# Performance work log

Measured on AMD Instinct MI355X. Metric: run time of the kernel, lower is better.

The kernel has to match this reference:

```python
import jax, jax.numpy as jnp
import numpy as np

D_MODEL = 1024
N_HEADS = 16
D_K = D_MODEL // N_HEADS
D_FF = 4096
EPS = 1e-6


def setup_inputs() -> dict:
    key = jax.random.key(0)
    ks = jax.random.split(key, 12)
    s = 1.0 / np.sqrt(D_MODEL)
    inp = {
        "x": jax.random.normal(ks[0], (4, 2048, D_MODEL), jnp.float32),
        "src_mask": jnp.ones((4, 1, 1, 2048), jnp.int32),
        "Wq": jax.random.normal(ks[1], (D_MODEL, D_MODEL), jnp.float32) * s,
        "bq": jnp.zeros((D_MODEL,), jnp.float32),
        "Wk": jax.random.normal(ks[2], (D_MODEL, D_MODEL), jnp.float32) * s,
        "bk": jnp.zeros((D_MODEL,), jnp.float32),
        "Wv": jax.random.normal(ks[3], (D_MODEL, D_MODEL), jnp.float32) * s,
        "bv": jnp.zeros((D_MODEL,), jnp.float32),
        "Wo": jax.random.normal(ks[4], (D_MODEL, D_MODEL), jnp.float32) * s,
        "bo": jnp.zeros((D_MODEL,), jnp.float32),
        "W1": jax.random.normal(ks[5], (D_MODEL, D_FF), jnp.float32) * s,
        "b1": jnp.zeros((D_FF,), jnp.float32),
        "W2": jax.random.normal(ks[6], (D_FF, D_MODEL), jnp.float32) * (1.0 / np.sqrt(D_FF)),
        "b2": jnp.zeros((D_MODEL,), jnp.float32),
        # scalar LayerNormalization params (alpha=ones(1), bias=zeros(1)) for the 2 residual norms
        "ln1_alpha": jnp.ones((1,), jnp.float32),
        "ln1_bias": jnp.zeros((1,), jnp.float32),
        "ln2_alpha": jnp.ones((1,), jnp.float32),
        "ln2_bias": jnp.zeros((1,), jnp.float32),
    }
    return inp


def _layernorm(x, alpha, bias):
    # matches torch: mean + std (unbiased, ddof=1), (x-mean)/(std+eps)
    mean = jnp.mean(x, axis=-1, keepdims=True)
    std = jnp.std(x, axis=-1, keepdims=True, ddof=1)
    return alpha * ((x - mean) / (std + EPS)) + bias


def _mha(x, mask, Wq, bq, Wk, bk, Wv, bv, Wo, bo):
    B, S, _ = x.shape
    q = (x @ Wq + bq).reshape(B, S, N_HEADS, D_K).transpose(0, 2, 1, 3)
    k = (x @ Wk + bk).reshape(B, S, N_HEADS, D_K).transpose(0, 2, 1, 3)
    v = (x @ Wv + bv).reshape(B, S, N_HEADS, D_K).transpose(0, 2, 1, 3)
    scores = jnp.einsum("bhqd,bhkd->bhqk", q, k) / jnp.sqrt(jnp.float32(D_K))
    scores = jnp.where(mask == 0, jnp.float32(-1e9), scores)
    attn = jax.nn.softmax(scores, axis=-1)
    ctx = jnp.einsum("bhqk,bhkd->bhqd", attn, v)
    ctx = ctx.transpose(0, 2, 1, 3).reshape(B, S, D_MODEL)
    return ctx @ Wo + bo


def reference(x, src_mask, Wq, bq, Wk, bk, Wv, bv, Wo, bo, W1, b1, W2, b2,
              ln1_alpha, ln1_bias, ln2_alpha, ln2_bias):
    # pre-norm residual 1: self-attention
    h = _layernorm(x, ln1_alpha, ln1_bias)
    x = x + _mha(h, src_mask, Wq, bq, Wk, bk, Wv, bv, Wo, bo)
    # pre-norm residual 2: FFN
    h = _layernorm(x, ln2_alpha, ln2_bias)
    ff = jax.nn.relu(h @ W1 + b1) @ W2 + b2
    return x + ff
```

## Files before the change

kernel.cpp:

```cpp
#include <hip/hip_runtime.h>

typedef __attribute__((ext_vector_type(8))) short v8s;
typedef __attribute__((ext_vector_type(4))) short v4s;
typedef __attribute__((ext_vector_type(8))) unsigned short v8u;
typedef __attribute__((ext_vector_type(4))) unsigned short v4u;
typedef __attribute__((ext_vector_type(4))) float f32x4;

#define DEV __device__ __forceinline__

DEV unsigned short f2bf(float f) {
  union { float f; unsigned u; } v; v.f = f;
  unsigned r = v.u + 0x7fffu + ((v.u >> 16) & 1u);
  return (unsigned short)(r >> 16);
}

DEV void gload16(const unsigned short* g, unsigned short* l) {
  __builtin_amdgcn_global_load_lds(
      (const __attribute__((address_space(1))) unsigned int*)g,
      (__attribute__((address_space(3))) unsigned int*)l, 16, 0, 0);
}

__global__ __launch_bounds__(256) void ln_kernel(
    const float* __restrict__ x, unsigned short* __restrict__ h,
    const float* __restrict__ alpha, const float* __restrict__ beta)
{
  int row = blockIdx.x;
  int tid = threadIdx.x;
  const float4* xr = reinterpret_cast<const float4*>(x + (size_t)row * 1024);
  float4 v = xr[tid];
  float s  = v.x + v.y + v.z + v.w;
  float ss = v.x * v.x + v.y * v.y + v.z * v.z + v.w * v.w;
#pragma unroll
  for (int off = 1; off < 64; off <<= 1) {
    s  += __shfl_xor(s, off);
    ss += __shfl_xor(ss, off);
  }
  __shared__ float ps[4][2];
  int wid = tid >> 6, lane = tid & 63;
  if (lane == 0) { ps[wid][0] = s; ps[wid][1] = ss; }
  __syncthreads();
  s  = ps[0][0] + ps[1][0] + ps[2][0] + ps[3][0];
  ss = ps[0][1] + ps[1][1] + ps[2][1] + ps[3][1];
  float mean = s * (1.0f / 1024.0f);
  float var  = (ss - 1024.0f * mean * mean) * (1.0f / 1023.0f);
  float inv  = 1.0f / (sqrtf(fmaxf(var, 0.0f)) + 1e-6f);
  float a = alpha[0], b = beta[0];
  v4u o;
  o[0] = f2bf(a * ((v.x - mean) * inv) + b);
  o[1] = f2bf(a * ((v.y - mean) * inv) + b);
  o[2] = f2bf(a * ((v.z - mean) * inv) + b);
  o[3] = f2bf(a * ((v.w - mean) * inv) + b);
  *reinterpret_cast<v4u*>(h + (size_t)row * 1024 + tid * 4) = o;
}

__global__ __launch_bounds__(256) void transpose_convert(
    const float* __restrict__ W, unsigned short* __restrict__ Wt, int K, int N)
{
  __shared__ float t[32][33];
  int n0 = blockIdx.x * 32, k0 = blockIdx.y * 32;
  int tx = threadIdx.x, ty = threadIdx.y;
#pragma unroll
  for (int i = 0; i < 4; ++i)
    t[ty + i * 8][tx] = W[(size_t)(k0 + ty + i * 8) * N + n0 + tx];
  __syncthreads();
#pragma unroll
  for (int i = 0; i < 4; ++i)
    Wt[(size_t)(n0 + ty + i * 8) * K + k0 + tx] = f2bf(t[tx][ty + i * 8]);
}

enum { MODE_QK = 0, MODE_VT = 1, MODE_RES = 2, MODE_FFN1 = 3 };

#define BUF_ELEMS ((128 + 256) * 64)

DEV void stage_part(const unsigned short* Aptr, const unsigned short* Bptr,
                    unsigned short* buf, int K, int part, int wid, int lane)
{
  {
    int d = (part * 8 + wid) * 64 + lane;
    int r = d >> 3, p = d & 7;
    gload16(Aptr + (size_t)r * K + 8 * (p ^ (r & 7)),
            buf + (size_t)(part * 8 + wid) * 512);
  }
#pragma unroll
  for (int j = 0; j < 2; ++j) {
    int ib = part * 2 + j;
    int d = (ib * 8 + wid) * 64 + lane;
    int r = d >> 3, p = d & 7;
    gload16(Bptr + (size_t)r * K + 8 * (p ^ (r & 7)),
            buf + 128 * 64 + (size_t)(ib * 8 + wid) * 512);
  }
}

template <int MODE>
__global__ __launch_bounds__(512, 2) void gemm_pipe(
    const unsigned short* __restrict__ A, const unsigned short* __restrict__ Bt,
    const float* __restrict__ bias, const float* __restrict__ resid,
    void* __restrict__ out, int M, int N, int K)
{
  __shared__ unsigned short lds[3 * BUF_ELEMS];

  int nbx = M >> 7, nwg = gridDim.x;
  int lin = blockIdx.x;
  int qq = nwg >> 3, rr = nwg & 7;
  int xcd = lin & 7, idx = lin >> 3;
  int swz = (xcd < rr ? xcd * (qq + 1) : rr * (qq + 1) + (xcd - rr) * qq) + idx;
  int bx = swz % nbx, by = swz / nbx;

  int tid = threadIdx.x, lane = tid & 63, wid = tid >> 6;
  int wm = wid >> 2, wn = wid & 3;
  int g = lane >> 4, c0 = lane & 15;
  int rowBase = bx * 128, colBase = by * 256;

  const unsigned short* Ab = A  + (size_t)rowBase * K;
  const unsigned short* Bb = Bt + (size_t)colBase * K;
  int NT = K >> 6;

  f32x4 acc[4][4];
#pragma unroll
  for (int m = 0; m < 4; ++m)
#pragma unroll
    for (int n = 0; n < 4; ++n) acc[m][n] = (f32x4){0.f, 0.f, 0.f, 0.f};

  stage_part(Ab, Bb, lds, K, 0, wid, lane);
  stage_part(Ab, Bb, lds, K, 1, wid, lane);
  stage_part(Ab + 64, Bb + 64, lds + BUF_ELEMS, K, 0, wid, lane);
  stage_part(Ab + 64, Bb + 64, lds + BUF_ELEMS, K, 1, wid, lane);
  asm volatile("s_waitcnt vmcnt(6)" ::: "memory");
  __builtin_amdgcn_s_barrier();
  asm volatile("" ::: "memory");

  int cur = 0;
  for (int t = 0; t < NT; ++t) {
    const char* Abuf = (const char*)(lds + cur * BUF_ELEMS);
    const char* Bbuf = Abuf + 128 * 128;
    int nxt2 = cur + 2; if (nxt2 >= 3) nxt2 -= 3;
    unsigned short* sbuf = lds + nxt2 * BUF_ELEMS;
    bool doStage = (t + 2 < NT);
    int ks = (t + 2) << 6;
    int e = (c0 & 7) << 4;

#pragma unroll
    for (int ph = 0; ph < 2; ++ph) {
      v8s af[4], bfr[4];
#pragma unroll
      for (int m = 0; m < 4; ++m)
        af[m] = *reinterpret_cast<const v8s*>(
            Abuf + (wm * 64 + m * 16 + c0) * 128 + ((ph * 64 + g * 16) ^ e));
#pragma unroll
      for (int n = 0; n < 4; ++n)
        bfr[n] = *reinterpret_cast<const v8s*>(
            Bbuf + (wn * 64 + n * 16 + c0) * 128 + ((ph * 64 + g * 16) ^ e));

      if (doStage) stage_part(Ab + ks, Bb + ks, sbuf, K, ph, wid, lane);

      __builtin_amdgcn_s_setprio(1);
#pragma unroll
      for (int m = 0; m < 4; ++m)
#pragma unroll
        for (int n = 0; n < 4; ++n)
          acc[m][n] = __builtin_amdgcn_mfma_f32_16x16x32_bf16(
              af[m], bfr[n], acc[m][n], 0, 0, 0);
      __builtin_amdgcn_s_setprio(0);

      if (ph == 1) {
        if (doStage) asm volatile("s_waitcnt vmcnt(6)" ::: "memory");
        else         asm volatile("s_waitcnt vmcnt(0)" ::: "memory");
      }
      __builtin_amdgcn_sched_barrier(0);
      __builtin_amdgcn_s_barrier();
      asm volatile("" ::: "memory");
    }
    cur = cur + 1; if (cur >= 3) cur -= 3;
  }

#pragma unroll
  for (int mf = 0; mf < 4; ++mf) {
#pragma unroll
    for (int n = 0; n < 4; ++n) {
#pragma unroll
      for (int r = 0; r < 4; ++r) {
        int row = rowBase + wm * 64 + mf * 16 + g * 4 + r;
        int col = colBase + wn * 64 + n * 16 + c0;
        float v = acc[mf][n][r] + bias[col];
        if constexpr (MODE == MODE_QK) {
          int b = row >> 11, sI = row & 2047, hh = col >> 6, d = col & 63;
          ((unsigned short*)out)[(((size_t)(b * 16 + hh)) * 2048 + sI) * 64 + d] = f2bf(v);
        } else if constexpr (MODE == MODE_VT) {
          int b = row >> 11, sI = row & 2047, hh = col >> 6, d = col & 63;
          ((unsigned short*)out)[(((size_t)(b * 16 + hh)) * 64 + d) * 2048 + sI] = f2bf(v);
        } else if constexpr (MODE == MODE_RES) {
          ((float*)out)[(size_t)row * N + col] = resid[(size_t)row * N + col] + v;
        } else {
          ((unsigned short*)out)[(size_t)row * N + col] = f2bf(fmaxf(v, 0.0f));
        }
      }
    }
  }
}

DEV void writeV(unsigned short* Vbuf, int idx, v8u vv) {
  int d = idx >> 3, k0 = (idx & 7) * 8;
  int slot0 = ((k0 >> 5) << 5) + (((k0 >> 2) & 3) << 3) + (((k0 >> 4) & 1) << 2);
  int b0 = (slot0 * 2) ^ ((d & 7) << 4);
  char* base = (char*)(Vbuf + d * 64);
  v4u lo = {vv[0], vv[1], vv[2], vv[3]};
  v4u hi = {vv[4], vv[5], vv[6], vv[7]};
  *reinterpret_cast<v4u*>(base + b0) = lo;
  *reinterpret_cast<v4u*>(base + (b0 ^ 16)) = hi;
}

__global__ __launch_bounds__(256) void attn_kernel(
    const unsigned short* __restrict__ q, const unsigned short* __restrict__ k,
    const unsigned short* __restrict__ vT, const int* __restrict__ mask,
    unsigned short* __restrict__ ctx)
{
  const int S = 2048, DK = 64, KVB = 64, NT = 32;
  const float SL2E = 0.125f * 1.44269504088896f;
  int bh = blockIdx.x;
  int b = bh >> 4, hh = bh & 15;
  int qbase = blockIdx.y * 64;
  int tid = threadIdx.x, lane = tid & 63, wid = tid >> 6;
  int g = lane >> 4, c0 = lane & 15;

  __shared__ unsigned short Ks[2][KVB * DK];
  __shared__ unsigned short Vs[2][DK * KVB];
  __shared__ float Msf[2][KVB];

  const unsigned short* qb = q  + (size_t)bh * S * DK;
  const unsigned short* kb = k  + (size_t)bh * S * DK;
  const unsigned short* vb = vT + (size_t)bh * DK * S;
  const int* mb = mask + b * S;

  int qrow = qbase + wid * 16 + c0;
  v8s aq[2];
#pragma unroll
  for (int t = 0; t < 2; ++t)
    aq[t] = *reinterpret_cast<const v8s*>(&qb[(size_t)qrow * DK + t * 32 + g * 8]);

  int i0 = tid, i1 = tid + 256;
  int r0 = i0 >> 3, m0 = i0 & 7;
  int r1 = i1 >> 3, m1 = i1 & 7;

  f32x4 acc[4];
#pragma unroll
  for (int no = 0; no < 4; ++no) acc[no] = (f32x4){0.f, 0.f, 0.f, 0.f};
  float mrow = -1e30f, lrow = 0.f;

  {
    gload16(kb + (size_t)r0 * DK + 8 * (m0 ^ (r0 & 7)), &Ks[0][i0 * 8]);
    gload16(kb + (size_t)r1 * DK + 8 * (m1 ^ (r1 & 7)), &Ks[0][i1 * 8]);
    v8u vv0 = *reinterpret_cast<const v8u*>(&vb[(size_t)r0 * S + m0 * 8]);
    v8u vv1 = *reinterpret_cast<const v8u*>(&vb[(size_t)r1 * S + m1 * 8]);
    writeV(Vs[0], i0, vv0);
    writeV(Vs[0], i1, vv1);
    if (tid < KVB) Msf[0][tid] = mb[tid] ? 0.f : -1e9f;
    __syncthreads();
  }

  for (int t = 0; t < NT; ++t) {
    int cur = t & 1, nxt = cur ^ 1;
    int ktn = (t + 1) * KVB;
    bool more = (t + 1 < NT);
    v8u vv0, vv1; float msv = 0.f;
    if (more) {
      gload16(kb + (size_t)(ktn + r0) * DK + 8 * (m0 ^ (r0 & 7)), &Ks[nxt][i0 * 8]);
      gload16(kb + (size_t)(ktn + r1) * DK + 8 * (m1 ^ (r1 & 7)), &Ks[nxt][i1 * 8]);
      vv0 = *reinterpret_cast<const v8u*>(&vb[(size_t)r0 * S + ktn + m0 * 8]);
      vv1 = *reinterpret_cast<const v8u*>(&vb[(size_t)r1 * S + ktn + m1 * 8]);
      if (tid < KVB) msv = mb[ktn + tid] ? 0.f : -1e9f;
    }

    float p[16];
#pragma unroll
    for (int n = 0; n < 4; ++n) {
      f32x4 sa = (f32x4){0.f, 0.f, 0.f, 0.f};
      int kvr = n * 16 + c0;
      const char* krow = (const char*)&Ks[cur][kvr * DK];
      int sw = (kvr & 7) << 4;
#pragma unroll
      for (int tt = 0; tt < 2; ++tt) {
        v8s ak = *reinterpret_cast<const v8s*>(krow + ((tt * 64 + g * 16) ^ sw));
        sa = __builtin_amdgcn_mfma_f32_16x16x32_bf16(ak, aq[tt], sa, 0, 0, 0);
      }
      f32x4 bn = *reinterpret_cast<const f32x4*>(&Msf[cur][n * 16 + g * 4]);
#pragma unroll
      for (int r = 0; r < 4; ++r) p[n * 4 + r] = sa[r] * SL2E + bn[r];
    }

    float pmax = p[0];
#pragma unroll
    for (int i = 1; i < 16; ++i) pmax = fmaxf(pmax, p[i]);
    pmax = fmaxf(pmax, __shfl_xor(pmax, 16));
    pmax = fmaxf(pmax, __shfl_xor(pmax, 32));
    if (!__all(pmax - mrow <= 8.0f)) {
      float mn = fmaxf(mrow, pmax);
      float sc = exp2f(mrow - mn);
      lrow *= sc;
#pragma unroll
      for (int no = 0; no < 4; ++no) {
        acc[no][0] *= sc; acc[no][1] *= sc; acc[no][2] *= sc; acc[no][3] *= sc;
      }
      mrow = mn;
    }
    float ts = 0.f;
#pragma unroll
    for (int i = 0; i < 16; ++i) { p[i] = exp2f(p[i] - mrow); ts += p[i]; }
    ts += __shfl_xor(ts, 16);
    ts += __shfl_xor(ts, 32);
    lrow += ts;

    v8s pbv[2];
#pragma unroll
    for (int c = 0; c < 2; ++c) {
      union { v8s s; unsigned u[4]; } pk;
#pragma unroll
      for (int hph = 0; hph < 4; ++hph)
        asm("v_cvt_pk_bf16_f32 %0, %1, %2"
            : "=v"(pk.u[hph]) : "v"(p[c * 8 + 2 * hph]), "v"(p[c * 8 + 2 * hph + 1]));
      pbv[c] = pk.s;
    }

#pragma unroll
    for (int c = 0; c < 2; ++c) {
#pragma unroll
      for (int no = 0; no < 4; ++no) {
        int d = no * 16 + c0;
        v8s av = *reinterpret_cast<const v8s*>(
            (const char*)&Vs[cur][d * 64] + ((c * 64 + g * 16) ^ ((d & 7) << 4)));
        acc[no] = __builtin_amdgcn_mfma_f32_16x16x32_bf16(av, pbv[c], acc[no], 0, 0, 0);
      }
    }

    if (more) {
      writeV(Vs[nxt], i0, vv0);
      writeV(Vs[nxt], i1, vv1);
      if (tid < KVB) Msf[nxt][tid] = msv;
    }
    __syncthreads();
  }

  float inv = 1.0f / fmaxf(lrow, 1e-20f);
#pragma unroll
  for (int no = 0; no < 4; ++no) {
    v4u o;
    o[0] = f2bf(acc[no][0] * inv);
    o[1] = f2bf(acc[no][1] * inv);
    o[2] = f2bf(acc[no][2] * inv);
    o[3] = f2bf(acc[no][3] * inv);
    *reinterpret_cast<v4u*>(
        &ctx[(size_t)(b * S + qrow) * 1024 + hh * 64 + no * 16 + g * 4]) = o;
  }
}

extern "C" void kernel_launch(void* const* d_in, const int* in_sizes, int n_in,
                              void* d_out, int out_size, void* d_ws, size_t ws_size,
                              hipStream_t stream)
{
  (void)in_sizes; (void)n_in; (void)out_size; (void)ws_size;
  const float* x    = (const float*)d_in[0];
  const int*   mask = (const int*)d_in[1];
  const float* Wq = (const float*)d_in[2];  const float* bq = (const float*)d_in[3];
  const float* Wk = (const float*)d_in[4];  const float* bk = (const float*)d_in[5];
  const float* Wv = (const float*)d_in[6];  const float* bv = (const float*)d_in[7];
  const float* Wo = (const float*)d_in[8];  const float* bo = (const float*)d_in[9];
  const float* W1 = (const float*)d_in[10]; const float* b1 = (const float*)d_in[11];
  const float* W2 = (const float*)d_in[12]; const float* b2 = (const float*)d_in[13];
  const float* ln1a = (const float*)d_in[14]; const float* ln1b = (const float*)d_in[15];
  const float* ln2a = (const float*)d_in[16]; const float* ln2b = (const float*)d_in[17];

  char* ws = (char*)d_ws;
  const size_t MB = (size_t)1 << 20;
  unsigned short* wqT = (unsigned short*)(ws + 0 * MB);
  unsigned short* wkT = (unsigned short*)(ws + 2 * MB);
  unsigned short* wvT = (unsigned short*)(ws + 4 * MB);
  unsigned short* woT = (unsigned short*)(ws + 6 * MB);
  unsigned short* w1T = (unsigned short*)(ws + 8 * MB);
  unsigned short* w2T = (unsigned short*)(ws + 16 * MB);
  unsigned short* hb  = (unsigned short*)(ws + 24 * MB);
  unsigned short* qb  = (unsigned short*)(ws + 40 * MB);
  unsigned short* kb  = (unsigned short*)(ws + 56 * MB);
  unsigned short* vTb = (unsigned short*)(ws + 72 * MB);
  unsigned short* ctx = (unsigned short*)(ws + 88 * MB);
  unsigned short* gb  = (unsigned short*)(ws + 40 * MB);
  float* xout = (float*)d_out;

  dim3 tb(32, 8);
  transpose_convert<<<dim3(32, 32),  tb, 0, stream>>>(Wq, wqT, 1024, 1024);
  transpose_convert<<<dim3(32, 32),  tb, 0, stream>>>(Wk, wkT, 1024, 1024);
  transpose_convert<<<dim3(32, 32),  tb, 0, stream>>>(Wv, wvT, 1024, 1024);
  transpose_convert<<<dim3(32, 32),  tb, 0, stream>>>(Wo, woT, 1024, 1024);
  transpose_convert<<<dim3(128, 32), tb, 0, stream>>>(W1, w1T, 1024, 4096);
  transpose_convert<<<dim3(32, 128), tb, 0, stream>>>(W2, w2T, 4096, 1024);

  ln_kernel<<<8192, 256, 0, stream>>>(x, hb, ln1a, ln1b);

  gemm_pipe<MODE_QK><<<256, 512, 0, stream>>>(hb, wqT, bq, nullptr, qb,  8192, 1024, 1024);
  gemm_pipe<MODE_QK><<<256, 512, 0, stream>>>(hb, wkT, bk, nullptr, kb,  8192, 1024, 1024);
  gemm_pipe<MODE_VT><<<256, 512, 0, stream>>>(hb, wvT, bv, nullptr, vTb, 8192, 1024, 1024);

  attn_kernel<<<dim3(64, 32), 256, 0, stream>>>(qb, kb, vTb, mask, ctx);

  gemm_pipe<MODE_RES><<<256, 512, 0, stream>>>(ctx, woT, bo, x, xout, 8192, 1024, 1024);

  ln_kernel<<<8192, 256, 0, stream>>>(xout, hb, ln2a, ln2b);

  gemm_pipe<MODE_FFN1><<<1024, 512, 0, stream>>>(hb, w1T, b1, nullptr, gb, 8192, 4096, 1024);
  gemm_pipe<MODE_RES><<<256, 512, 0, stream>>>(gb, w2T, b2, xout, xout, 8192, 1024, 4096);
}
```

Measured before the change: 448.7 us.

## Fuse QKV projections, switch GEMMs to 4-stage ring, pre-pack V and fold softmax scale

Replaces the three Q/K/V GEMMs with one fused GEMM over a concatenated weight, using a new 4-deep ring-buffered GEMM with K-step 32 and optional 256-row tiles for the QKV and FFN1 GEMMs. The QKV epilogue folds the softmax scale into Q and writes V in a pre-swizzled per-tile layout, so attention can load V straight into LDS with async loads instead of register shuffles. Attention also skips mask arithmetic when a whole 64-key tile is unmasked. Larger tiles raise register pressure and the epilogue scatter is more complex.

```diff
diff --git a/kernel.cpp b/kernel.cpp
--- a/kernel.cpp
+++ b/kernel.cpp
@@ -1,7 +1,6 @@
 #include <hip/hip_runtime.h>
 
 typedef __attribute__((ext_vector_type(8))) short v8s;
-typedef __attribute__((ext_vector_type(4))) short v4s;
 typedef __attribute__((ext_vector_type(8))) unsigned short v8u;
 typedef __attribute__((ext_vector_type(4))) unsigned short v4u;
 typedef __attribute__((ext_vector_type(4))) float f32x4;
@@ -19,6 +18,8 @@
       (const __attribute__((address_space(1))) unsigned int*)g,
       (__attribute__((address_space(3))) unsigned int*)l, 16, 0, 0);
 }
+
+#define SL2E 0.1803368801111204f
 
 __global__ __launch_bounds__(256) void ln_kernel(
     const float* __restrict__ x, unsigned short* __restrict__ h,
@@ -68,38 +69,25 @@
     Wt[(size_t)(n0 + ty + i * 8) * K + k0 + tx] = f2bf(t[tx][ty + i * 8]);
 }
 
-enum { MODE_QK = 0, MODE_VT = 1, MODE_RES = 2, MODE_FFN1 = 3 };
-
-#define BUF_ELEMS ((128 + 256) * 64)
-
-DEV void stage_part(const unsigned short* Aptr, const unsigned short* Bptr,
-                    unsigned short* buf, int K, int part, int wid, int lane)
+enum { MODE_QKV = 0, MODE_RES = 2, MODE_FFN1 = 3 };
+
+template <int MODE, int BM>
+__global__ __launch_bounds__(512, 2) void gemm_ring(
+    const unsigned short* __restrict__ A, const unsigned short* __restrict__ Bt,
+    const float* __restrict__ bias0, const float* __restrict__ bias1,
+    const float* __restrict__ bias2, const float* __restrict__ resid,
+    void* __restrict__ o0, void* __restrict__ o1, void* __restrict__ o2,
+    int M, int N, int K)
 {
-  {
-    int d = (part * 8 + wid) * 64 + lane;
-    int r = d >> 3, p = d & 7;
-    gload16(Aptr + (size_t)r * K + 8 * (p ^ (r & 7)),
-            buf + (size_t)(part * 8 + wid) * 512);
-  }
-#pragma unroll
-  for (int j = 0; j < 2; ++j) {
-    int ib = part * 2 + j;
-    int d = (ib * 8 + wid) * 64 + lane;
-    int r = d >> 3, p = d & 7;
-    gload16(Bptr + (size_t)r * K + 8 * (p ^ (r & 7)),
-            buf + 128 * 64 + (size_t)(ib * 8 + wid) * 512);
-  }
-}
-
-template <int MODE>
-__global__ __launch_bounds__(512, 2) void gemm_pipe(
-    const unsigned short* __restrict__ A, const unsigned short* __restrict__ Bt,
-    const float* __restrict__ bias, const float* __restrict__ resid,
-    void* __restrict__ out, int M, int N, int K)
-{
-  __shared__ unsigned short lds[3 * BUF_ELEMS];
-
-  int nbx = M >> 7, nwg = gridDim.x;
+  constexpr int MF = (BM == 256) ? 8 : 4;
+  constexpr int CA = BM / 128;
+  constexpr int LOADS = CA + 2;
+  constexpr int AELEMS = BM * 32;
+  constexpr int BUFE = (BM + 256) * 32;
+  constexpr int WROWS = BM / 2;
+  __shared__ unsigned short lds[4 * BUFE];
+
+  int nbx = M / BM, nwg = gridDim.x;
   int lin = blockIdx.x;
   int qq = nwg >> 3, rr = nwg & 7;
   int xcd = lin & 7, idx = lin >> 3;
@@ -109,126 +97,144 @@
   int tid = threadIdx.x, lane = tid & 63, wid = tid >> 6;
   int wm = wid >> 2, wn = wid & 3;
   int g = lane >> 4, c0 = lane & 15;
-  int rowBase = bx * 128, colBase = by * 256;
+  int rowBase = bx * BM, colBase = by * 256;
 
   const unsigned short* Ab = A  + (size_t)rowBase * K;
   const unsigned short* Bb = Bt + (size_t)colBase * K;
-  int NT = K >> 6;
-
-  f32x4 acc[4][4];
-#pragma unroll
-  for (int m = 0; m < 4; ++m)
+  int NT = K >> 5;
+
+  const unsigned short* srcA[CA]; int dqA[CA];
+  const unsigned short* srcB[2];  int dqB[2];
+#pragma unroll
+  for (int c = 0; c < CA; ++c) {
+    int qg = c * 512 + wid * 64 + lane;
+    int rp = qg >> 3, u = (qg & 7) ^ (rp & 7);
+    srcA[c] = Ab + (size_t)(2 * rp + (u >> 2)) * K + (u & 3) * 8;
+    dqA[c] = qg;
+  }
+#pragma unroll
+  for (int c = 0; c < 2; ++c) {
+    int qg = c * 512 + wid * 64 + lane;
+    int rp = qg >> 3, u = (qg & 7) ^ (rp & 7);
+    srcB[c] = Bb + (size_t)(2 * rp + (u >> 2)) * K + (u & 3) * 8;
+    dqB[c] = qg;
+  }
+
+  int u = ((c0 & 1) * 4 + g) ^ ((c0 >> 1) & 7);
+  int abase = (wm * (WROWS / 2) + (c0 >> 1)) * 128 + u * 16;
+  int bbase = (wn * 32 + (c0 >> 1)) * 128 + u * 16 + AELEMS * 2;
+
+  f32x4 acc[MF][4];
+#pragma unroll
+  for (int m = 0; m < MF; ++m)
 #pragma unroll
     for (int n = 0; n < 4; ++n) acc[m][n] = (f32x4){0.f, 0.f, 0.f, 0.f};
 
-  stage_part(Ab, Bb, lds, K, 0, wid, lane);
-  stage_part(Ab, Bb, lds, K, 1, wid, lane);
-  stage_part(Ab + 64, Bb + 64, lds + BUF_ELEMS, K, 0, wid, lane);
-  stage_part(Ab + 64, Bb + 64, lds + BUF_ELEMS, K, 1, wid, lane);
-  asm volatile("s_waitcnt vmcnt(6)" ::: "memory");
+#define STAGE(tt) do { \
+    unsigned short* sb_ = lds + ((tt) & 3) * BUFE; int ks_ = (tt) << 5; \
+    _Pragma("unroll") for (int c = 0; c < CA; ++c) gload16(srcA[c] + ks_, sb_ + dqA[c] * 8); \
+    _Pragma("unroll") for (int c = 0; c < 2;  ++c) gload16(srcB[c] + ks_, sb_ + AELEMS + dqB[c] * 8); \
+  } while (0)
+
+  STAGE(0); STAGE(1); STAGE(2);
+  if constexpr (LOADS == 4) asm volatile("s_waitcnt vmcnt(8)" ::: "memory");
+  else                      asm volatile("s_waitcnt vmcnt(6)" ::: "memory");
   __builtin_amdgcn_s_barrier();
   asm volatile("" ::: "memory");
 
-  int cur = 0;
   for (int t = 0; t < NT; ++t) {
-    const char* Abuf = (const char*)(lds + cur * BUF_ELEMS);
-    const char* Bbuf = Abuf + 128 * 128;
-    int nxt2 = cur + 2; if (nxt2 >= 3) nxt2 -= 3;
-    unsigned short* sbuf = lds + nxt2 * BUF_ELEMS;
-    bool doStage = (t + 2 < NT);
-    int ks = (t + 2) << 6;
-    int e = (c0 & 7) << 4;
-
-#pragma unroll
-    for (int ph = 0; ph < 2; ++ph) {
-      v8s af[4], bfr[4];
-#pragma unroll
-      for (int m = 0; m < 4; ++m)
-        af[m] = *reinterpret_cast<const v8s*>(
-            Abuf + (wm * 64 + m * 16 + c0) * 128 + ((ph * 64 + g * 16) ^ e));
+    const char* buf = (const char*)(lds + (t & 3) * BUFE);
+    v8s af[MF], bfr[4];
+#pragma unroll
+    for (int m = 0; m < MF; ++m)
+      af[m] = *reinterpret_cast<const v8s*>(buf + abase + m * 1024);
+#pragma unroll
+    for (int n = 0; n < 4; ++n)
+      bfr[n] = *reinterpret_cast<const v8s*>(buf + bbase + n * 1024);
+
+    bool s3 = (t + 3 < NT);
+    if (s3) STAGE(t + 3);
+
+    __builtin_amdgcn_s_setprio(1);
+#pragma unroll
+    for (int m = 0; m < MF; ++m)
 #pragma unroll
       for (int n = 0; n < 4; ++n)
-        bfr[n] = *reinterpret_cast<const v8s*>(
-            Bbuf + (wn * 64 + n * 16 + c0) * 128 + ((ph * 64 + g * 16) ^ e));
-
-      if (doStage) stage_part(Ab + ks, Bb + ks, sbuf, K, ph, wid, lane);
-
-      __builtin_amdgcn_s_setprio(1);
-#pragma unroll
-      for (int m = 0; m < 4; ++m)
-#pragma unroll
-        for (int n = 0; n < 4; ++n)
-          acc[m][n] = __builtin_amdgcn_mfma_f32_16x16x32_bf16(
-              af[m], bfr[n], acc[m][n], 0, 0, 0);
-      __builtin_amdgcn_s_setprio(0);
-
-      if (ph == 1) {
-        if (doStage) asm volatile("s_waitcnt vmcnt(6)" ::: "memory");
-        else         asm volatile("s_waitcnt vmcnt(0)" ::: "memory");
-      }
-      __builtin_amdgcn_sched_barrier(0);
-      __builtin_amdgcn_s_barrier();
-      asm volatile("" ::: "memory");
-    }
-    cur = cur + 1; if (cur >= 3) cur -= 3;
-  }
-
-#pragma unroll
-  for (int mf = 0; mf < 4; ++mf) {
-#pragma unroll
-    for (int n = 0; n < 4; ++n) {
+        acc[m][n] = __builtin_amdgcn_mfma_f32_16x16x32_bf16(af[m], bfr[n], acc[m][n], 0, 0, 0);
+    __builtin_amdgcn_s_setprio(0);
+
+    if (s3) {
+      if constexpr (LOADS == 4) asm volatile("s_waitcnt vmcnt(8)" ::: "memory");
+      else                      asm volatile("s_waitcnt vmcnt(6)" ::: "memory");
+    } else if (t + 2 < NT) {
+      if constexpr (LOADS == 4) asm volatile("s_waitcnt vmcnt(4)" ::: "memory");
+      else                      asm volatile("s_waitcnt vmcnt(3)" ::: "memory");
+    } else if (t + 1 < NT) {
+      asm volatile("s_waitcnt vmcnt(0)" ::: "memory");
+    }
+    __builtin_amdgcn_sched_barrier(0);
+    __builtin_amdgcn_s_barrier();
+    asm volatile("" ::: "memory");
+  }
+#undef STAGE
+
+#pragma unroll
+  for (int mf = 0; mf < MF; ++mf) {
+#pragma unroll
+    for (int nf = 0; nf < 4; ++nf) {
 #pragma unroll
       for (int r = 0; r < 4; ++r) {
-        int row = rowBase + wm * 64 + mf * 16 + g * 4 + r;
-        int col = colBase + wn * 64 + n * 16 + c0;
-        float v = acc[mf][n][r] + bias[col];
-        if constexpr (MODE == MODE_QK) {
-          int b = row >> 11, sI = row & 2047, hh = col >> 6, d = col & 63;
-          ((unsigned short*)out)[(((size_t)(b * 16 + hh)) * 2048 + sI) * 64 + d] = f2bf(v);
-        } else if constexpr (MODE == MODE_VT) {
-          int b = row >> 11, sI = row & 2047, hh = col >> 6, d = col & 63;
-          ((unsigned short*)out)[(((size_t)(b * 16 + hh)) * 64 + d) * 2048 + sI] = f2bf(v);
+        int row = rowBase + wm * WROWS + mf * 16 + g * 4 + r;
+        int col = colBase + wn * 64 + nf * 16 + c0;
+        if constexpr (MODE == MODE_QKV) {
+          int sect = colBase >> 10;
+          int cs = col & 1023;
+          const float* bp = sect == 0 ? bias0 : (sect == 1 ? bias1 : bias2);
+          float v = acc[mf][nf][r] + bp[cs];
+          int hh = cs >> 6, d = cs & 63;
+          int b = row >> 11, sI = row & 2047;
+          size_t bh = (size_t)(b * 16 + hh);
+          if (sect == 0) {
+            ((unsigned short*)o0)[(bh * 2048 + sI) * 64 + d] = f2bf(v * SL2E);
+          } else if (sect == 1) {
+            ((unsigned short*)o1)[(bh * 2048 + sI) * 64 + d] = f2bf(v);
+          } else {
+            int k6 = sI & 63;
+            int slot = ((k6 >> 5) << 5) | (((k6 >> 2) & 3) << 3) |
+                       (((k6 >> 4) & 1) << 2) | (k6 & 3);
+            int e = slot ^ ((d & 7) << 3);
+            ((unsigned short*)o2)[((bh * 32 + (sI >> 6)) * 64 + d) * 64 + e] = f2bf(v);
+          }
         } else if constexpr (MODE == MODE_RES) {
-          ((float*)out)[(size_t)row * N + col] = resid[(size_t)row * N + col] + v;
+          float v = acc[mf][nf][r] + bias0[col];
+          ((float*)o0)[(size_t)row * N + col] = resid[(size_t)row * N + col] + v;
         } else {
-          ((unsigned short*)out)[(size_t)row * N + col] = f2bf(fmaxf(v, 0.0f));
+          float v = acc[mf][nf][r] + bias0[col];
+          ((unsigned short*)o0)[(size_t)row * N + col] = f2bf(fmaxf(v, 0.0f));
         }
       }
     }
   }
 }
 
-DEV void writeV(unsigned short* Vbuf, int idx, v8u vv) {
-  int d = idx >> 3, k0 = (idx & 7) * 8;
-  int slot0 = ((k0 >> 5) << 5) + (((k0 >> 2) & 3) << 3) + (((k0 >> 4) & 1) << 2);
-  int b0 = (slot0 * 2) ^ ((d & 7) << 4);
-  char* base = (char*)(Vbuf + d * 64);
-  v4u lo = {vv[0], vv[1], vv[2], vv[3]};
-  v4u hi = {vv[4], vv[5], vv[6], vv[7]};
-  *reinterpret_cast<v4u*>(base + b0) = lo;
-  *reinterpret_cast<v4u*>(base + (b0 ^ 16)) = hi;
-}
-
 __global__ __launch_bounds__(256) void attn_kernel(
     const unsigned short* __restrict__ q, const unsigned short* __restrict__ k,
-    const unsigned short* __restrict__ vT, const int* __restrict__ mask,
+    const unsigned short* __restrict__ vP, const int* __restrict__ mask,
     unsigned short* __restrict__ ctx)
 {
-  const int S = 2048, DK = 64, KVB = 64, NT = 32;
-  const float SL2E = 0.125f * 1.44269504088896f;
+  const int S = 2048, DK = 64, NT = 32;
   int bh = blockIdx.x;
   int b = bh >> 4, hh = bh & 15;
   int qbase = blockIdx.y * 64;
   int tid = threadIdx.x, lane = tid & 63, wid = tid >> 6;
   int g = lane >> 4, c0 = lane & 15;
 
-  __shared__ unsigned short Ks[2][KVB * DK];
-  __shared__ unsigned short Vs[2][DK * KVB];
-  __shared__ float Msf[2][KVB];
-
-  const unsigned short* qb = q  + (size_t)bh * S * DK;
-  const unsigned short* kb = k  + (size_t)bh * S * DK;
-  const unsigned short* vb = vT + (size_t)bh * DK * S;
+  __shared__ unsigned short Ks[2][4096];
+  __shared__ unsigned short Vs[2][4096];
+
+  const unsigned short* qb  = q  + (size_t)bh * S * DK;
+  const unsigned short* kb  = k  + (size_t)bh * S * DK;
+  const unsigned short* vPb = vP + (size_t)bh * 32 * 4096;
   const int* mb = mask + b * S;
 
   int qrow = qbase + wid * 16 + c0;
@@ -240,35 +246,31 @@
   int i0 = tid, i1 = tid + 256;
   int r0 = i0 >> 3, m0 = i0 & 7;
   int r1 = i1 >> 3, m1 = i1 & 7;
+  const unsigned short* ks0 = kb + (size_t)r0 * DK + 8 * (m0 ^ (r0 & 7));
+  const unsigned short* ks1 = kb + (size_t)r1 * DK + 8 * (m1 ^ (r1 & 7));
 
   f32x4 acc[4];
 #pragma unroll
   for (int no = 0; no < 4; ++no) acc[no] = (f32x4){0.f, 0.f, 0.f, 0.f};
   float mrow = -1e30f, lrow = 0.f;
 
-  {
-    gload16(kb + (size_t)r0 * DK + 8 * (m0 ^ (r0 & 7)), &Ks[0][i0 * 8]);
-    gload16(kb + (size_t)r1 * DK + 8 * (m1 ^ (r1 & 7)), &Ks[0][i1 * 8]);
-    v8u vv0 = *reinterpret_cast<const v8u*>(&vb[(size_t)r0 * S + m0 * 8]);
-    v8u vv1 = *reinterpret_cast<const v8u*>(&vb[(size_t)r1 * S + m1 * 8]);
-    writeV(Vs[0], i0, vv0);
-    writeV(Vs[0], i1, vv1);
-    if (tid < KVB) Msf[0][tid] = mb[tid] ? 0.f : -1e9f;
-    __syncthreads();
-  }
+  gload16(ks0, &Ks[0][i0 * 8]);
+  gload16(ks1, &Ks[0][i1 * 8]);
+  gload16(vPb + i0 * 8, &Vs[0][i0 * 8]);
+  gload16(vPb + i1 * 8, &Vs[0][i1 * 8]);
+  __syncthreads();
 
   for (int t = 0; t < NT; ++t) {
     int cur = t & 1, nxt = cur ^ 1;
-    int ktn = (t + 1) * KVB;
-    bool more = (t + 1 < NT);
-    v8u vv0, vv1; float msv = 0.f;
-    if (more) {
-      gload16(kb + (size_t)(ktn + r0) * DK + 8 * (m0 ^ (r0 & 7)), &Ks[nxt][i0 * 8]);
-      gload16(kb + (size_t)(ktn + r1) * DK + 8 * (m1 ^ (r1 & 7)), &Ks[nxt][i1 * 8]);
-      vv0 = *reinterpret_cast<const v8u*>(&vb[(size_t)r0 * S + ktn + m0 * 8]);
-      vv1 = *reinterpret_cast<const v8u*>(&vb[(size_t)r1 * S + ktn + m1 * 8]);
-      if (tid < KVB) msv = mb[ktn + tid] ? 0.f : -1e9f;
-    }
+    if (t + 1 < NT) {
+      int kofs = (t + 1) * 64 * DK;
+      gload16(ks0 + kofs, &Ks[nxt][i0 * 8]);
+      gload16(ks1 + kofs, &Ks[nxt][i1 * 8]);
+      gload16(vPb + (t + 1) * 4096 + i0 * 8, &Vs[nxt][i0 * 8]);
+      gload16(vPb + (t + 1) * 4096 + i1 * 8, &Vs[nxt][i1 * 8]);
+    }
+    int mv = mb[t * 64 + lane];
+    bool allv = __all(mv != 0);
 
     float p[16];
 #pragma unroll
@@ -282,9 +284,18 @@
         v8s ak = *reinterpret_cast<const v8s*>(krow + ((tt * 64 + g * 16) ^ sw));
         sa = __builtin_amdgcn_mfma_f32_16x16x32_bf16(ak, aq[tt], sa, 0, 0, 0);
       }
-      f32x4 bn = *reinterpret_cast<const f32x4*>(&Msf[cur][n * 16 + g * 4]);
-#pragma unroll
-      for (int r = 0; r < 4; ++r) p[n * 4 + r] = sa[r] * SL2E + bn[r];
+#pragma unroll
+      for (int r = 0; r < 4; ++r) p[n * 4 + r] = sa[r];
+    }
+    if (!allv) {
+#pragma unroll
+      for (int n = 0; n < 4; ++n) {
+        int4 mm = *reinterpret_cast<const int4*>(&mb[t * 64 + n * 16 + g * 4]);
+        p[n * 4 + 0] += mm.x ? 0.f : -1e9f;
+        p[n * 4 + 1] += mm.y ? 0.f : -1e9f;
+        p[n * 4 + 2] += mm.z ? 0.f : -1e9f;
+        p[n * 4 + 3] += mm.w ? 0.f : -1e9f;
+      }
     }
 
     float pmax = p[0];
@@ -329,12 +340,6 @@
             (const char*)&Vs[cur][d * 64] + ((c * 64 + g * 16) ^ ((d & 7) << 4)));
         acc[no] = __builtin_amdgcn_mfma_f32_16x16x32_bf16(av, pbv[c], acc[no], 0, 0, 0);
       }
-    }
-
-    if (more) {
-      writeV(Vs[nxt], i0, vv0);
-      writeV(Vs[nxt], i1, vv1);
-      if (tid < KVB) Msf[nxt][tid] = msv;
     }
     __syncthreads();
   }
@@ -370,40 +375,41 @@
 
   char* ws = (char*)d_ws;
   const size_t MB = (size_t)1 << 20;
-  unsigned short* wqT = (unsigned short*)(ws + 0 * MB);
-  unsigned short* wkT = (unsigned short*)(ws + 2 * MB);
-  unsigned short* wvT = (unsigned short*)(ws + 4 * MB);
+  unsigned short* wqkvT = (unsigned short*)(ws + 0 * MB);
   unsigned short* woT = (unsigned short*)(ws + 6 * MB);
   unsigned short* w1T = (unsigned short*)(ws + 8 * MB);
   unsigned short* w2T = (unsigned short*)(ws + 16 * MB);
   unsigned short* hb  = (unsigned short*)(ws + 24 * MB);
   unsigned short* qb  = (unsigned short*)(ws + 40 * MB);
   unsigned short* kb  = (unsigned short*)(ws + 56 * MB);
-  unsigned short* vTb = (unsigned short*)(ws + 72 * MB);
+  unsigned short* vPb = (unsigned short*)(ws + 72 * MB);
   unsigned short* ctx = (unsigned short*)(ws + 88 * MB);
   unsigned short* gb  = (unsigned short*)(ws + 40 * MB);
   float* xout = (float*)d_out;
 
   dim3 tb(32, 8);
-  transpose_convert<<<dim3(32, 32),  tb, 0, stream>>>(Wq, wqT, 1024, 1024);
-  transpose_convert<<<dim3(32, 32),  tb, 0, stream>>>(Wk, wkT, 1024, 1024);
-  transpose_convert<<<dim3(32, 32),  tb, 0, stream>>>(Wv, wvT, 1024, 1024);
+  transpose_convert<<<dim3(32, 32),  tb, 0, stream>>>(Wq, wqkvT,                 1024, 1024);
+  transpose_convert<<<dim3(32, 32),  tb, 0, stream>>>(Wk, wqkvT + 1024 * 1024,   1024, 1024);
+  transpose_convert<<<dim3(32, 32),  tb, 0, stream>>>(Wv, wqkvT + 2048 * 1024,   1024, 1024);
   transpose_convert<<<dim3(32, 32),  tb, 0, stream>>>(Wo, woT, 1024, 1024);
   transpose_convert<<<dim3(128, 32), tb, 0, stream>>>(W1, w1T, 1024, 4096);
   transpose_convert<<<dim3(32, 128), tb, 0, stream>>>(W2, w2T, 4096, 1024);
 
   ln_kernel<<<8192, 256, 0, stream>>>(x, hb, ln1a, ln1b);
 
-  gemm_pipe<MODE_QK><<<256, 512, 0, stream>>>(hb, wqT, bq, nullptr, qb,  8192, 1024, 1024);
-  gemm_pipe<MODE_QK><<<256, 512, 0, stream>>>(hb, wkT, bk, nullptr, kb,  8192, 1024, 1024);
-  gemm_pipe<MODE_VT><<<256, 512, 0, stream>>>(hb, wvT, bv, nullptr, vTb, 8192, 1024, 1024);
-
-  attn_kernel<<<dim3(64, 32), 256, 0, stream>>>(qb, kb, vTb, mask, ctx);
-
-  gemm_pipe<MODE_RES><<<256, 512, 0, stream>>>(ctx, woT, bo, x, xout, 8192, 1024, 1024);
+  gemm_ring<MODE_QKV, 256><<<384, 512, 0, stream>>>(
+      hb, wqkvT, bq, bk, bv, nullptr, qb, kb, vPb, 8192, 3072, 1024);
+
+  attn_kernel<<<dim3(64, 32), 256, 0, stream>>>(qb, kb, vPb, mask, ctx);
+
+  gemm_ring<MODE_RES, 128><<<256, 512, 0, stream>>>(
+      ctx, woT, bo, nullptr, nullptr, x, xout, nullptr, nullptr, 8192, 1024, 1024);
 
   ln_kernel<<<8192, 256, 0, stream>>>(xout, hb, ln2a, ln2b);
 
-  gemm_pipe<MODE_FFN1><<<1024, 512, 0, stream>>>(hb, w1T, b1, nullptr, gb, 8192, 4096, 1024);
-  gemm_pipe<MODE_RES><<<256, 512, 0, stream>>>(gb, w2T, b2, xout, xout, 8192, 1024, 4096);
-}
+  gemm_ring<MODE_FFN1, 256><<<512, 512, 0, stream>>>(
+      hb, w1T, b1, nullptr, nullptr, nullptr, gb, nullptr, nullptr, 8192, 4096, 1024);
+
+  gemm_ring<MODE_RES, 128><<<256, 512, 0, stream>>>(
+      gb, w2T, b2, nullptr, nullptr, xout, xout, nullptr, nullptr, 8192, 1024, 4096);
+}
```

New measurement: 464.6 us. 3.6% more time.
